# Optimization experiments

Measured on AMD Instinct MI355X. Metric: run time of the kernel, lower is better.

The kernel has to match this reference:

```python
import jax, jax.numpy as jnp
import numpy as np

H = 512
S = 65  # 64 board cells + appended constant 1


def _heads(y, wk, wq, wv):
    # y: [H, S]; wk/wq/wv: [3, H, H] -> atts: [3, S, H]
    def one(wk_i, wq_i, wv_i):
        k = wk_i @ y            # [H, S]
        q = wq_i @ y            # [H, S]
        v = wv_i @ y            # [H, S]
        sm = jax.nn.softmax(k.T @ q, axis=1)  # [S, S], softmax over dim=1
        return sm @ v.T         # [S, H]
    return jax.vmap(one)(wk, wq, wv)


def setup_inputs() -> dict:
    key = jax.random.key(0)
    ks = jax.random.split(key, 10)
    r = lambda k, s: jax.random.normal(k, s, dtype=jnp.float32)
    return {
        "inputs": r(ks[0], (1, 64)),
        "embedding": r(ks[1], (H, S)),
        "wq": r(ks[2], (3, 3, H, H)),
        "wk": r(ks[3], (3, 3, H, H)),
        "wv": r(ks[4], (3, 3, H, H)),
        "linear1": r(ks[5], (3 * H, H)),
        "linear2": r(ks[6], (3 * H, H)),
        "linear3": r(ks[7], (3 * H, 2 * H)),
        "linear4": r(ks[8], (2 * H, H)),
        "linear5": r(ks[9], (H, 64)),
    }


def reference(inputs, embedding, wq, wk, wv, linear1, linear2, linear3, linear4, linear5):
    x = jnp.concatenate([inputs[0], jnp.ones((1,), inputs.dtype)])  # [S]
    y = embedding * x  # [H, S] (broadcast over rows)

    # Layer 1 (3 heads)
    a1 = _heads(y, wk[0], wq[0], wv[0])  # [3, S, H]
    y = jax.nn.relu(jnp.concatenate([a1[0], a1[1], a1[2]], axis=1) @ linear1).T  # [H, S]

    # Layer 2 -- NOTE: original code cats att11, att12, att23 (a bug we preserve)
    a2 = _heads(y, wk[1], wq[1], wv[1])
    y = jax.nn.relu(jnp.concatenate([a1[0], a1[1], a2[2]], axis=1) @ linear2).T  # [H, S]

    # Layer 3 -- NOTE: original code cats att11, att12, att33 (preserved)
    a3 = _heads(y, wk[2], wq[2], wv[2])
    y = jax.nn.relu(jnp.concatenate([a1[0], a1[1], a3[2]], axis=1) @ linear3)[64]  # [2H]

    # dropout p=0.1 -> identity in eval mode
    y = jnp.tanh(y @ linear4)  # [H]
    score = y @ linear5        # [64]
    return score[None, :]      # [1, 64]
```

## Files before the change

### kernel.cpp

```cpp
#include <hip/hip_runtime.h>
#include <hip/hip_bf16.h>
#include <math.h>

#define H 512
#define S 65
#define SP 80
#define HS (H * S)
#define PHS (H * SP)
#define KS3 24
#define KS4 16


__global__ void scale_embed_kernel(const float* __restrict__ inp,
                                   const float* __restrict__ emb,
                                   float* __restrict__ yT) {
    int i = blockIdx.x * blockDim.x + threadIdx.x;
    if (i < PHS) {
        int s = i / H;
        int h = i % H;
        float v = 0.0f;
        if (s < S) {
            float x = (s == 64) ? 1.0f : inp[s];
            v = emb[h * S + s] * x;
        }
        yT[i] = v;
    }
}

__global__ void __launch_bounds__(256, 2)
kqv_gemm_tiled(const float* __restrict__ wq,
               const float* __restrict__ wk,
               const float* __restrict__ wv,
               int layer, int head0,
               const float* __restrict__ yT,
               float* __restrict__ part) {
    int slot  = blockIdx.z;
    int which = blockIdx.y;
    int mat = layer * 3 + head0 + slot;
    const float* W = (which == 0 ? wk : (which == 1 ? wq : wv)) + (size_t)mat * H * H;

    int n0   = (blockIdx.x & 7) * 64;
    int kidx = blockIdx.x >> 3;

    __shared__ float Wt[64 * 64];
    __shared__ float As[SP * 64];

    int t  = threadIdx.x;
    int nq = t & 15;
    int g  = t >> 4;

    float4 acc[5];
#pragma unroll
    for (int r = 0; r < 5; ++r) acc[r] = make_float4(0.f, 0.f, 0.f, 0.f);

    for (int ch = 0; ch < 4; ++ch) {
        int kc0 = kidx * 256 + ch * 64;

#pragma unroll
        for (int c = 0; c < 4; ++c) {
            int f = c * 256 + t;
            int wn  = f >> 4;
            int kf4 = f & 15;
            float4 w4 = *(const float4*)(W + (size_t)(n0 + wn) * H + kc0 + 4 * kf4);
            int sw = ((wn >> 2) ^ (kf4 & 7));
            int base = (4 * kf4) * 64 + 4 * sw + (wn & 3);
            Wt[base      ] = w4.x;
            Wt[base +  64] = w4.y;
            Wt[base + 128] = w4.z;
            Wt[base + 192] = w4.w;
        }
#pragma unroll
        for (int c = 0; c < 5; ++c) {
            int f = c * 256 + t;
            int as  = f >> 4;
            int kf4 = f & 15;
            *(float4*)(&As[as * 64 + 4 * kf4]) =
                *(const float4*)(yT + (size_t)as * H + kc0 + 4 * kf4);
        }
        __syncthreads();

#pragma unroll
        for (int k4 = 0; k4 < 16; ++k4) {
            int swc = 4 * (nq ^ (k4 & 7));
            float4 w0 = *(const float4*)(&Wt[(4 * k4 + 0) * 64 + swc]);
            float4 w1 = *(const float4*)(&Wt[(4 * k4 + 1) * 64 + swc]);
            float4 w2 = *(const float4*)(&Wt[(4 * k4 + 2) * 64 + swc]);
            float4 w3 = *(const float4*)(&Wt[(4 * k4 + 3) * 64 + swc]);
#pragma unroll
            for (int r = 0; r < 5; ++r) {
                float4 a = *(const float4*)(&As[(g + 16 * r) * 64 + 4 * k4]);
                acc[r].x = fmaf(a.x, w0.x, acc[r].x);
                acc[r].y = fmaf(a.x, w0.y, acc[r].y);
                acc[r].z = fmaf(a.x, w0.z, acc[r].z);
                acc[r].w = fmaf(a.x, w0.w, acc[r].w);
                acc[r].x = fmaf(a.y, w1.x, acc[r].x);
                acc[r].y = fmaf(a.y, w1.y, acc[r].y);
                acc[r].z = fmaf(a.y, w1.z, acc[r].z);
                acc[r].w = fmaf(a.y, w1.w, acc[r].w);
                acc[r].x = fmaf(a.z, w2.x, acc[r].x);
                acc[r].y = fmaf(a.z, w2.y, acc[r].y);
                acc[r].z = fmaf(a.z, w2.z, acc[r].z);
                acc[r].w = fmaf(a.z, w2.w, acc[r].w);
                acc[r].x = fmaf(a.w, w3.x, acc[r].x);
                acc[r].y = fmaf(a.w, w3.y, acc[r].y);
                acc[r].z = fmaf(a.w, w3.z, acc[r].z);
                acc[r].w = fmaf(a.w, w3.w, acc[r].w);
            }
        }
        __syncthreads();
    }

    float* P = part + (size_t)((slot * 3 + which) * 2 + kidx) * PHS;
#pragma unroll
    for (int r = 0; r < 5; ++r) {
        *(float4*)(P + (size_t)(g + 16 * r) * H + n0 + 4 * nq) = acc[r];
    }
}

__global__ void attn_kernel(const float* __restrict__ kqvp,
                            float* __restrict__ att) {
    int a = blockIdx.x;
    int slot = blockIdx.y;
    int tid = threadIdx.x;

    const float* K0 = kqvp + (size_t)(slot * 3 + 0) * 2 * PHS;
    const float* K1 = K0 + PHS;
    const float* Q0 = kqvp + (size_t)(slot * 3 + 1) * 2 * PHS;
    const float* Q1 = Q0 + PHS;
    const float* V0 = kqvp + (size_t)(slot * 3 + 2) * 2 * PHS;
    const float* V1 = V0 + PHS;
    float* ao = att + (size_t)slot * S * H;

    __shared__ float ka[H];
    __shared__ float smv[S];
    __shared__ float p[S];

    ka[tid]       = K0[(size_t)a * H + tid]       + K1[(size_t)a * H + tid];
    ka[tid + 256] = K0[(size_t)a * H + tid + 256] + K1[(size_t)a * H + tid + 256];
    __syncthreads();

    if (tid < S) {
        const float4* q0 = (const float4*)(Q0 + (size_t)tid * H);
        const float4* q1 = (const float4*)(Q1 + (size_t)tid * H);
        const float4* kl = (const float4*)ka;
        float4 c0 = {0,0,0,0}, c1 = {0,0,0,0};
        for (int t = 0; t < H / 4; t += 2) {
            float4 qa = q0[t],     qb = q1[t];
            float4 qc = q0[t + 1], qd = q1[t + 1];
            float4 k0 = kl[t], k1 = kl[t + 1];
            c0.x = fmaf(k0.x, qa.x + qb.x, c0.x);
            c0.y = fmaf(k0.y, qa.y + qb.y, c0.y);
            c0.z = fmaf(k0.z, qa.z + qb.z, c0.z);
            c0.w = fmaf(k0.w, qa.w + qb.w, c0.w);
            c1.x = fmaf(k1.x, qc.x + qd.x, c1.x);
            c1.y = fmaf(k1.y, qc.y + qd.y, c1.y);
            c1.z = fmaf(k1.z, qc.z + qd.z, c1.z);
            c1.w = fmaf(k1.w, qc.w + qd.w, c1.w);
        }
        smv[tid] = ((c0.x + c0.y) + (c0.z + c0.w)) + ((c1.x + c1.y) + (c1.z + c1.w));
    }
    __syncthreads();

    float maxv = -INFINITY;
    for (int i = 0; i < S; ++i) maxv = fmaxf(maxv, smv[i]);
    float sum = 0.0f;
    for (int i = 0; i < S; ++i) sum += expf(smv[i] - maxv);
    float inv = 1.0f / sum;
    if (tid < S) p[tid] = expf(smv[tid] - maxv) * inv;
    __syncthreads();

#pragma unroll
    for (int rep = 0; rep < 2; ++rep) {
        int hh = tid + rep * 256;
        float a0 = 0.f, a1 = 0.f;
#pragma unroll 4
        for (int b = 0; b < 64; b += 2) {
            a0 = fmaf(p[b    ], V0[(size_t)(b    ) * H + hh] + V1[(size_t)(b    ) * H + hh], a0);
            a1 = fmaf(p[b + 1], V0[(size_t)(b + 1) * H + hh] + V1[(size_t)(b + 1) * H + hh], a1);
        }
        a0 = fmaf(p[64], V0[(size_t)64 * H + hh] + V1[(size_t)64 * H + hh], a0);
        ao[(size_t)a * H + hh] = a0 + a1;
    }
}

__global__ void linA_kernel(const float* __restrict__ att1,
                            const float* __restrict__ lin1,
                            const float* __restrict__ lin2,
                            float* __restrict__ part1,
                            float* __restrict__ part2) {
    int seg = blockIdx.y;
    int i = blockIdx.x * blockDim.x + threadIdx.x;
    int s = i / H;
    int h = i % H;

    const float* att;
    const float* L;
    float* dst;
    if (seg < 6) {
        att = att1 + (size_t)(seg >> 1) * HS;
        L   = lin1 + (size_t)(seg * 256) * H + h;
        dst = part1 + (size_t)seg * HS;
    } else {
        int s2 = seg - 6;
        att = att1 + (size_t)(s2 >> 1) * HS;
        L   = lin2 + (size_t)(s2 * 256) * H + h;
        dst = part2 + (size_t)s2 * HS;
    }
    const float* row = att + (size_t)s * H + (seg & 1) * 256;

    float a0 = 0.f, a1 = 0.f, a2 = 0.f, a3 = 0.f;
    for (int j = 0; j < 256; j += 4) {
        a0 = fmaf(row[j + 0], L[(size_t)(j + 0) * H], a0);
        a1 = fmaf(row[j + 1], L[(size_t)(j + 1) * H], a1);
        a2 = fmaf(row[j + 2], L[(size_t)(j + 2) * H], a2);
        a3 = fmaf(row[j + 3], L[(size_t)(j + 3) * H], a3);
    }
    dst[i] = (a0 + a1) + (a2 + a3);
}

__global__ void lin2c_kernel(const float* __restrict__ att2,
                             const float* __restrict__ lin2,
                             float* __restrict__ part2) {
    int seg = 4 + blockIdx.y;
    int i = blockIdx.x * blockDim.x + threadIdx.x;
    int s = i / H;
    int h = i % H;

    const float* row = att2 + (size_t)s * H + (seg & 1) * 256;
    const float* L = lin2 + (size_t)(seg * 256) * H + h;

    float a0 = 0.f, a1 = 0.f, a2 = 0.f, a3 = 0.f;
    for (int j = 0; j < 256; j += 4) {
        a0 = fmaf(row[j + 0], L[(size_t)(j + 0) * H], a0);
        a1 = fmaf(row[j + 1], L[(size_t)(j + 1) * H], a1);
        a2 = fmaf(row[j + 2], L[(size_t)(j + 2) * H], a2);
        a3 = fmaf(row[j + 3], L[(size_t)(j + 3) * H], a3);
    }
    part2[(size_t)seg * HS + i] = (a0 + a1) + (a2 + a3);
}

__global__ void combine_relu_kernel(const float* __restrict__ part,
                                    float* __restrict__ yT) {
    int i = blockIdx.x * blockDim.x + threadIdx.x;
    if (i >= HS) return;
    float s = part[i] + part[HS + i] + part[2 * HS + i]
            + part[3 * HS + i] + part[4 * HS + i] + part[5 * HS + i];
    yT[i] = fmaxf(s, 0.0f);
}

__global__ void lin3ab_kernel(const float* __restrict__ att1,
                              const float* __restrict__ lin3,
                              float* __restrict__ tpart) {
    int j2 = blockIdx.x * 256 + threadIdx.x;
    int ks = blockIdx.y;
    const float* row = att1 + (size_t)(ks >> 3) * HS + (size_t)64 * H;
    int j0 = (ks & 7) * 64;
    int jbase = ks * 64;

    float a0 = 0.f, a1 = 0.f, a2 = 0.f, a3 = 0.f;
    for (int j = 0; j < 64; j += 4) {
        a0 = fmaf(row[j0 + j + 0], lin3[(size_t)(jbase + j + 0) * 1024 + j2], a0);
        a1 = fmaf(row[j0 + j + 1], lin3[(size_t)(jbase + j + 1) * 1024 + j2], a1);
        a2 = fmaf(row[j0 + j + 2], lin3[(size_t)(jbase + j + 2) * 1024 + j2], a2);
        a3 = fmaf(row[j0 + j + 3], lin3[(size_t)(jbase + j + 3) * 1024 + j2], a3);
    }
    tpart[ks * 1024 + j2] = (a0 + a1) + (a2 + a3);
}

__global__ void attn3_lin3c_kernel(const float* __restrict__ kqvp,
                                   const float* __restrict__ lin3,
                                   float* __restrict__ tpart) {
    int tid = threadIdx.x;
    int ks  = 16 + blockIdx.y;
    int j2  = blockIdx.x * 256 + tid;
    int j0  = (ks & 7) * 64;

    const float* K0 = kqvp;
    const float* K1 = kqvp + PHS;
    const float* Q0 = kqvp + 2 * (size_t)PHS;
    const float* Q1 = kqvp + 3 * (size_t)PHS;
    const float* V0 = kqvp + 4 * (size_t)PHS;
    const float* V1 = kqvp + 5 * (size_t)PHS;

    __shared__ float ka[H];
    __shared__ float smv[S];
    __shared__ float p[S];
    __shared__ float att_s[64];

    ka[tid]       = K0[(size_t)64 * H + tid]       + K1[(size_t)64 * H + tid];
    ka[tid + 256] = K0[(size_t)64 * H + tid + 256] + K1[(size_t)64 * H + tid + 256];
    __syncthreads();

    if (tid < S) {
        const float4* q0 = (const float4*)(Q0 + (size_t)tid * H);
        const float4* q1 = (const float4*)(Q1 + (size_t)tid * H);
        const float4* kl = (const float4*)ka;
        float4 c0 = {0,0,0,0}, c1 = {0,0,0,0};
        for (int t = 0; t < H / 4; t += 2) {
            float4 qa = q0[t],     qb = q1[t];
            float4 qc = q0[t + 1], qd = q1[t + 1];
            float4 k0 = kl[t], k1 = kl[t + 1];
            c0.x = fmaf(k0.x, qa.x + qb.x, c0.x);
            c0.y = fmaf(k0.y, qa.y + qb.y, c0.y);
            c0.z = fmaf(k0.z, qa.z + qb.z, c0.z);
            c0.w = fmaf(k0.w, qa.w + qb.w, c0.w);
            c1.x = fmaf(k1.x, qc.x + qd.x, c1.x);
            c1.y = fmaf(k1.y, qc.y + qd.y, c1.y);
            c1.z = fmaf(k1.z, qc.z + qd.z, c1.z);
            c1.w = fmaf(k1.w, qc.w + qd.w, c1.w);
        }
        smv[tid] = ((c0.x + c0.y) + (c0.z + c0.w)) + ((c1.x + c1.y) + (c1.z + c1.w));
    }
    __syncthreads();

    float maxv = -INFINITY;
    for (int i = 0; i < S; ++i) maxv = fmaxf(maxv, smv[i]);
    float sum = 0.0f;
    for (int i = 0; i < S; ++i) sum += expf(smv[i] - maxv);
    float inv = 1.0f / sum;
    if (tid < S) p[tid] = expf(smv[tid] - maxv) * inv;
    __syncthreads();

    if (tid < 64) {
        int hh = j0 + tid;
        float a0 = 0.f, a1 = 0.f;
#pragma unroll 4
        for (int b = 0; b < 64; b += 2) {
            a0 = fmaf(p[b    ], V0[(size_t)(b    ) * H + hh] + V1[(size_t)(b    ) * H + hh], a0);
            a1 = fmaf(p[b + 1], V0[(size_t)(b + 1) * H + hh] + V1[(size_t)(b + 1) * H + hh], a1);
        }
        a0 = fmaf(p[64], V0[(size_t)64 * H + hh] + V1[(size_t)64 * H + hh], a0);
        att_s[tid] = a0 + a1;
    }
    __syncthreads();

    int jbase = ks * 64;
    float a0 = 0.f, a1 = 0.f, a2 = 0.f, a3 = 0.f;
    for (int j = 0; j < 64; j += 4) {
        a0 = fmaf(att_s[j + 0], lin3[(size_t)(jbase + j + 0) * 1024 + j2], a0);
        a1 = fmaf(att_s[j + 1], lin3[(size_t)(jbase + j + 1) * 1024 + j2], a1);
        a2 = fmaf(att_s[j + 2], lin3[(size_t)(jbase + j + 2) * 1024 + j2], a2);
        a3 = fmaf(att_s[j + 3], lin3[(size_t)(jbase + j + 3) * 1024 + j2], a3);
    }
    tpart[ks * 1024 + j2] = (a0 + a1) + (a2 + a3);
}

__global__ void lin4_partial_kernel(const float* __restrict__ tpart,
                                    const float* __restrict__ lin4,
                                    float* __restrict__ upart) {
    __shared__ float tl[64];
    int hh = blockIdx.x * 256 + threadIdx.x;
    int ks = blockIdx.y;
    int j2base = ks * 64;

    if (threadIdx.x < 64) {
        int j2 = j2base + threadIdx.x;
        float s = 0.f;
#pragma unroll
        for (int p = 0; p < KS3; ++p) s += tpart[p * 1024 + j2];
        tl[threadIdx.x] = fmaxf(s, 0.f);
    }
    __syncthreads();

    float a0 = 0.f, a1 = 0.f, a2 = 0.f, a3 = 0.f;
    for (int j = 0; j < 64; j += 4) {
        a0 = fmaf(tl[j + 0], lin4[(size_t)(j2base + j + 0) * H + hh], a0);
        a1 = fmaf(tl[j + 1], lin4[(size_t)(j2base + j + 1) * H + hh], a1);
        a2 = fmaf(tl[j + 2], lin4[(size_t)(j2base + j + 2) * H + hh], a2);
        a3 = fmaf(tl[j + 3], lin4[(size_t)(j2base + j + 3) * H + hh], a3);
    }
    upart[ks * H + hh] = (a0 + a1) + (a2 + a3);
}

__global__ void final_out_kernel(const float* __restrict__ upart,
                                 const float* __restrict__ lin5,
                                 float* __restrict__ out) {
    __shared__ float u[H];
    __shared__ float pr[8][64];
    int tid = threadIdx.x;

    {
        float s = 0.f;
#pragma unroll
        for (int p = 0; p < KS4; ++p) s += upart[p * H + tid];
        u[tid] = tanhf(s);
    }
    __syncthreads();

    int o  = tid & 63;
    int sl = tid >> 6;
    float acc = 0.f;
    int h0 = sl * 64;
#pragma unroll 8
    for (int j = 0; j < 64; ++j) {
        acc = fmaf(u[h0 + j], lin5[(h0 + j) * 64 + o], acc);
    }
    pr[sl][o] = acc;
    __syncthreads();

    if (tid < 64) {
        float s = 0.f;
#pragma unroll
        for (int p = 0; p < 8; ++p) s += pr[p][tid];
        out[tid] = s;
    }
}

extern "C" void kernel_launch(void* const* d_in, const int* in_sizes, int n_in,
                              void* d_out, int out_size, void* d_ws, size_t ws_size,
                              hipStream_t stream) {
    const float* inputs  = (const float*)d_in[0];
    const float* emb     = (const float*)d_in[1];
    const float* wq      = (const float*)d_in[2];
    const float* wk      = (const float*)d_in[3];
    const float* wv      = (const float*)d_in[4];
    const float* linear1 = (const float*)d_in[5];
    const float* linear2 = (const float*)d_in[6];
    const float* linear3 = (const float*)d_in[7];
    const float* linear4 = (const float*)d_in[8];
    const float* linear5 = (const float*)d_in[9];
    float* out = (float*)d_out;

    float* ws    = (float*)d_ws;
    float* y     = ws;
    float* kqvp  = y     + PHS;
    float* att1  = kqvp  + 18 * PHS;
    float* att2  = att1  + 3 * HS;
    float* part1 = att2  + HS;
    float* part2 = part1 + 6 * HS;
    float* tpart = part2 + 6 * HS;
    float* upart = tpart + KS3 * 1024;

    const int nb  = HS / 256;
    const int nbp = PHS / 256;

    scale_embed_kernel<<<nbp, 256, 0, stream>>>(inputs, emb, y);

    kqv_gemm_tiled<<<dim3(16, 3, 3), 256, 0, stream>>>(wq, wk, wv, 0, 0, y, kqvp);
    attn_kernel<<<dim3(S, 3), 256, 0, stream>>>(kqvp, att1);
    linA_kernel<<<dim3(nb, 10), 256, 0, stream>>>(att1, linear1, linear2, part1, part2);
    lin3ab_kernel<<<dim3(4, 16), 256, 0, stream>>>(att1, linear3, tpart);
    combine_relu_kernel<<<nb, 256, 0, stream>>>(part1, y);

    kqv_gemm_tiled<<<dim3(16, 3, 1), 256, 0, stream>>>(wq, wk, wv, 1, 2, y, kqvp);
    attn_kernel<<<dim3(S, 1), 256, 0, stream>>>(kqvp, att2);
    lin2c_kernel<<<dim3(nb, 2), 256, 0, stream>>>(att2, linear2, part2);
    combine_relu_kernel<<<nb, 256, 0, stream>>>(part2, y);

    kqv_gemm_tiled<<<dim3(16, 3, 1), 256, 0, stream>>>(wq, wk, wv, 2, 2, y, kqvp);
    attn3_lin3c_kernel<<<dim3(4, 8), 256, 0, stream>>>(kqvp, linear3, tpart);

    lin4_partial_kernel<<<dim3(2, KS4), 256, 0, stream>>>(tpart, linear4, upart);
    final_out_kernel<<<1, 512, 0, stream>>>(upart, linear5, out);
}
```

Baseline: 262.2 us.

## Replace naive linear-layer kernels with shared-memory tiled GEMM and parallelize attention scores

The per-element linear1/linear2 kernels, which streamed a weight column per thread, are replaced by a shared-memory tiled GEMM that uses 64x64 weight tiles, 80-row activation tiles and register blocking, split-K into 12 partials. The lin3ab work is folded into the linear1 launch, and the combine step now sums 12 padded partials. The attention score dot products are split across all 256 threads (4 slices per key) rather than only 65 threads. This trades a larger partial-sum buffer and an extra reduction for better weight reuse and higher thread utilization.

```diff
diff --git a/kernel.cpp b/kernel.cpp
--- a/kernel.cpp
+++ b/kernel.cpp
@@ -18,7 +18,7 @@
     if (i < PHS) {
         int s = i / H;
         int h = i % H;
-        float v = 0.0f;
+        float v = 0.f;
         if (s < S) {
             float x = (s == 64) ? 1.0f : inp[s];
             v = emb[h * S + s] * x;
@@ -55,7 +55,6 @@
 
     for (int ch = 0; ch < 4; ++ch) {
         int kc0 = kidx * 256 + ch * 64;
-
 #pragma unroll
         for (int c = 0; c < 4; ++c) {
             int f = c * 256 + t;
@@ -117,21 +116,47 @@
     }
 }
 
+__device__ __forceinline__ float score_part(const float* __restrict__ Q0,
+                                            const float* __restrict__ Q1,
+                                            const float* __restrict__ ka,
+                                            int b, int t) {
+    const float4* q0 = (const float4*)(Q0 + (size_t)b * H) + t * 32;
+    const float4* q1 = (const float4*)(Q1 + (size_t)b * H) + t * 32;
+    const float4* kl = (const float4*)ka + t * 32;
+    float4 c0 = {0,0,0,0}, c1 = {0,0,0,0};
+#pragma unroll
+    for (int u = 0; u < 32; u += 2) {
+        float4 qa = q0[u], qb = q1[u], k0 = kl[u];
+        float4 qc = q0[u+1], qd = q1[u+1], k1 = kl[u+1];
+        c0.x = fmaf(k0.x, qa.x + qb.x, c0.x);
+        c0.y = fmaf(k0.y, qa.y + qb.y, c0.y);
+        c0.z = fmaf(k0.z, qa.z + qb.z, c0.z);
+        c0.w = fmaf(k0.w, qa.w + qb.w, c0.w);
+        c1.x = fmaf(k1.x, qc.x + qd.x, c1.x);
+        c1.y = fmaf(k1.y, qc.y + qd.y, c1.y);
+        c1.z = fmaf(k1.z, qc.z + qd.z, c1.z);
+        c1.w = fmaf(k1.w, qc.w + qd.w, c1.w);
+    }
+    return ((c0.x + c0.y) + (c0.z + c0.w)) + ((c1.x + c1.y) + (c1.z + c1.w));
+}
+
 __global__ void attn_kernel(const float* __restrict__ kqvp,
                             float* __restrict__ att) {
     int a = blockIdx.x;
     int slot = blockIdx.y;
     int tid = threadIdx.x;
 
-    const float* K0 = kqvp + (size_t)(slot * 3 + 0) * 2 * PHS;
-    const float* K1 = K0 + PHS;
-    const float* Q0 = kqvp + (size_t)(slot * 3 + 1) * 2 * PHS;
-    const float* Q1 = Q0 + PHS;
-    const float* V0 = kqvp + (size_t)(slot * 3 + 2) * 2 * PHS;
-    const float* V1 = V0 + PHS;
-    float* ao = att + (size_t)slot * S * H;
+    const float* base = kqvp + (size_t)slot * 6 * PHS;
+    const float* K0 = base;
+    const float* K1 = base + PHS;
+    const float* Q0 = base + 2 * (size_t)PHS;
+    const float* Q1 = base + 3 * (size_t)PHS;
+    const float* V0 = base + 4 * (size_t)PHS;
+    const float* V1 = base + 5 * (size_t)PHS;
+    float* ao = att + (size_t)slot * PHS + (size_t)a * H;
 
     __shared__ float ka[H];
+    __shared__ float sp[4 * 65];
     __shared__ float smv[S];
     __shared__ float p[S];
 
@@ -139,25 +164,16 @@
     ka[tid + 256] = K0[(size_t)a * H + tid + 256] + K1[(size_t)a * H + tid + 256];
     __syncthreads();
 
+    {
+        int b = tid & 63;
+        int t = tid >> 6;
+        sp[t * 65 + b] = score_part(Q0, Q1, ka, b, t);
+        if (tid < 4) sp[tid * 65 + 64] = score_part(Q0, Q1, ka, 64, tid);
+    }
+    __syncthreads();
+
     if (tid < S) {
-        const float4* q0 = (const float4*)(Q0 + (size_t)tid * H);
-        const float4* q1 = (const float4*)(Q1 + (size_t)tid * H);
-        const float4* kl = (const float4*)ka;
-        float4 c0 = {0,0,0,0}, c1 = {0,0,0,0};
-        for (int t = 0; t < H / 4; t += 2) {
-            float4 qa = q0[t],     qb = q1[t];
-            float4 qc = q0[t + 1], qd = q1[t + 1];
-            float4 k0 = kl[t], k1 = kl[t + 1];
-            c0.x = fmaf(k0.x, qa.x + qb.x, c0.x);
-            c0.y = fmaf(k0.y, qa.y + qb.y, c0.y);
-            c0.z = fmaf(k0.z, qa.z + qb.z, c0.z);
-            c0.w = fmaf(k0.w, qa.w + qb.w, c0.w);
-            c1.x = fmaf(k1.x, qc.x + qd.x, c1.x);
-            c1.y = fmaf(k1.y, qc.y + qd.y, c1.y);
-            c1.z = fmaf(k1.z, qc.z + qd.z, c1.z);
-            c1.w = fmaf(k1.w, qc.w + qd.w, c1.w);
-        }
-        smv[tid] = ((c0.x + c0.y) + (c0.z + c0.w)) + ((c1.x + c1.y) + (c1.z + c1.w));
+        smv[tid] = (sp[tid] + sp[65 + tid]) + (sp[130 + tid] + sp[195 + tid]);
     }
     __syncthreads();
 
@@ -179,92 +195,149 @@
             a1 = fmaf(p[b + 1], V0[(size_t)(b + 1) * H + hh] + V1[(size_t)(b + 1) * H + hh], a1);
         }
         a0 = fmaf(p[64], V0[(size_t)64 * H + hh] + V1[(size_t)64 * H + hh], a0);
-        ao[(size_t)a * H + hh] = a0 + a1;
-    }
-}
-
-__global__ void linA_kernel(const float* __restrict__ att1,
-                            const float* __restrict__ lin1,
-                            const float* __restrict__ lin2,
-                            float* __restrict__ part1,
-                            float* __restrict__ part2) {
-    int seg = blockIdx.y;
-    int i = blockIdx.x * blockDim.x + threadIdx.x;
-    int s = i / H;
-    int h = i % H;
-
-    const float* att;
-    const float* L;
-    float* dst;
-    if (seg < 6) {
-        att = att1 + (size_t)(seg >> 1) * HS;
-        L   = lin1 + (size_t)(seg * 256) * H + h;
-        dst = part1 + (size_t)seg * HS;
+        ao[hh] = a0 + a1;
+    }
+}
+
+__device__ __forceinline__ void lin_gemm_dev(const float* __restrict__ A01,
+                                             const float* __restrict__ A2,
+                                             const float* __restrict__ L,
+                                             float* __restrict__ Pbase,
+                                             int ntile, int kidx, int kbase,
+                                             int tid,
+                                             float* __restrict__ Bs,
+                                             float* __restrict__ As) {
+    int n0 = ntile * 64;
+    int nq = tid & 15;
+    int g  = tid >> 4;
+
+    float4 acc[5];
+#pragma unroll
+    for (int r = 0; r < 5; ++r) acc[r] = make_float4(0.f, 0.f, 0.f, 0.f);
+
+#pragma unroll
+    for (int ch = 0; ch < 2; ++ch) {
+        int kg = kbase + kidx * 128 + ch * 64;
+        int head = kg >> 9;
+        const float* Asrc = (head < 2) ? (A01 + (size_t)head * PHS) : A2;
+        int col0 = kg & 511;
+
+#pragma unroll
+        for (int c = 0; c < 4; ++c) {
+            int f = c * 256 + tid;
+            int kk  = f >> 4;
+            int hf4 = f & 15;
+            *(float4*)(&Bs[kk * 64 + 4 * hf4]) =
+                *(const float4*)(L + (size_t)(kg + kk) * H + n0 + 4 * hf4);
+        }
+#pragma unroll
+        for (int c = 0; c < 5; ++c) {
+            int f = c * 256 + tid;
+            int as  = f >> 4;
+            int kf4 = f & 15;
+            *(float4*)(&As[as * 68 + 4 * kf4]) =
+                *(const float4*)(Asrc + (size_t)as * H + col0 + 4 * kf4);
+        }
+        __syncthreads();
+
+#pragma unroll
+        for (int k4 = 0; k4 < 16; ++k4) {
+            float4 w0 = *(const float4*)(&Bs[(4 * k4 + 0) * 64 + 4 * nq]);
+            float4 w1 = *(const float4*)(&Bs[(4 * k4 + 1) * 64 + 4 * nq]);
+            float4 w2 = *(const float4*)(&Bs[(4 * k4 + 2) * 64 + 4 * nq]);
+            float4 w3 = *(const float4*)(&Bs[(4 * k4 + 3) * 64 + 4 * nq]);
+#pragma unroll
+            for (int r = 0; r < 5; ++r) {
+                float4 a = *(const float4*)(&As[(g + 16 * r) * 68 + 4 * k4]);
+                acc[r].x = fmaf(a.x, w0.x, acc[r].x);
+                acc[r].y = fmaf(a.x, w0.y, acc[r].y);
+                acc[r].z = fmaf(a.x, w0.z, acc[r].z);
+                acc[r].w = fmaf(a.x, w0.w, acc[r].w);
+                acc[r].x = fmaf(a.y, w1.x, acc[r].x);
+                acc[r].y = fmaf(a.y, w1.y, acc[r].y);
+                acc[r].z = fmaf(a.y, w1.z, acc[r].z);
+                acc[r].w = fmaf(a.y, w1.w, acc[r].w);
+                acc[r].x = fmaf(a.z, w2.x, acc[r].x);
+                acc[r].y = fmaf(a.z, w2.y, acc[r].y);
+                acc[r].z = fmaf(a.z, w2.z, acc[r].z);
+                acc[r].w = fmaf(a.z, w2.w, acc[r].w);
+                acc[r].x = fmaf(a.w, w3.x, acc[r].x);
+                acc[r].y = fmaf(a.w, w3.y, acc[r].y);
+                acc[r].z = fmaf(a.w, w3.z, acc[r].z);
+                acc[r].w = fmaf(a.w, w3.w, acc[r].w);
+            }
+        }
+        __syncthreads();
+    }
+
+    float* P = Pbase + (size_t)kidx * PHS;
+#pragma unroll
+    for (int r = 0; r < 5; ++r) {
+        *(float4*)(P + (size_t)(g + 16 * r) * H + n0 + 4 * nq) = acc[r];
+    }
+}
+
+__global__ void __launch_bounds__(256, 2)
+lin1plus_kernel(const float* __restrict__ att1,
+                const float* __restrict__ lin1,
+                const float* __restrict__ lin3,
+                float* __restrict__ plin1,
+                float* __restrict__ tpart) {
+    __shared__ float Bs[64 * 64];
+    __shared__ float As[SP * 68];
+    int bx = blockIdx.x;
+    int tid = threadIdx.x;
+
+    if (bx < 96) {
+        lin_gemm_dev(att1, att1 + 2 * (size_t)PHS, lin1, plin1,
+                     bx & 7, bx >> 3, 0, tid, Bs, As);
     } else {
-        int s2 = seg - 6;
-        att = att1 + (size_t)(s2 >> 1) * HS;
-        L   = lin2 + (size_t)(s2 * 256) * H + h;
-        dst = part2 + (size_t)s2 * HS;
-    }
-    const float* row = att + (size_t)s * H + (seg & 1) * 256;
-
-    float a0 = 0.f, a1 = 0.f, a2 = 0.f, a3 = 0.f;
-    for (int j = 0; j < 256; j += 4) {
-        a0 = fmaf(row[j + 0], L[(size_t)(j + 0) * H], a0);
-        a1 = fmaf(row[j + 1], L[(size_t)(j + 1) * H], a1);
-        a2 = fmaf(row[j + 2], L[(size_t)(j + 2) * H], a2);
-        a3 = fmaf(row[j + 3], L[(size_t)(j + 3) * H], a3);
-    }
-    dst[i] = (a0 + a1) + (a2 + a3);
-}
-
-__global__ void lin2c_kernel(const float* __restrict__ att2,
-                             const float* __restrict__ lin2,
-                             float* __restrict__ part2) {
-    int seg = 4 + blockIdx.y;
-    int i = blockIdx.x * blockDim.x + threadIdx.x;
-    int s = i / H;
-    int h = i % H;
-
-    const float* row = att2 + (size_t)s * H + (seg & 1) * 256;
-    const float* L = lin2 + (size_t)(seg * 256) * H + h;
-
-    float a0 = 0.f, a1 = 0.f, a2 = 0.f, a3 = 0.f;
-    for (int j = 0; j < 256; j += 4) {
-        a0 = fmaf(row[j + 0], L[(size_t)(j + 0) * H], a0);
-        a1 = fmaf(row[j + 1], L[(size_t)(j + 1) * H], a1);
-        a2 = fmaf(row[j + 2], L[(size_t)(j + 2) * H], a2);
-        a3 = fmaf(row[j + 3], L[(size_t)(j + 3) * H], a3);
-    }
-    part2[(size_t)seg * HS + i] = (a0 + a1) + (a2 + a3);
-}
-
-__global__ void combine_relu_kernel(const float* __restrict__ part,
-                                    float* __restrict__ yT) {
-    int i = blockIdx.x * blockDim.x + threadIdx.x;
-    if (i >= HS) return;
-    float s = part[i] + part[HS + i] + part[2 * HS + i]
-            + part[3 * HS + i] + part[4 * HS + i] + part[5 * HS + i];
+        int idx = bx - 96;
+        int j2 = (idx & 3) * 256 + tid;
+        int ks = idx >> 2;
+        const float* row = att1 + (size_t)(ks >> 3) * PHS + (size_t)64 * H;
+        int j0 = (ks & 7) * 64;
+        int jbase = ks * 64;
+        float a0 = 0.f, a1 = 0.f, a2 = 0.f, a3 = 0.f;
+        for (int j = 0; j < 64; j += 4) {
+            a0 = fmaf(row[j0 + j + 0], lin3[(size_t)(jbase + j + 0) * 1024 + j2], a0);
+            a1 = fmaf(row[j0 + j + 1], lin3[(size_t)(jbase + j + 1) * 1024 + j2], a1);
+            a2 = fmaf(row[j0 + j + 2], lin3[(size_t)(jbase + j + 2) * 1024 + j2], a2);
+            a3 = fmaf(row[j0 + j + 3], lin3[(size_t)(jbase + j + 3) * 1024 + j2], a3);
+        }
+        tpart[ks * 1024 + j2] = (a0 + a1) + (a2 + a3);
+    }
+}
+
+__global__ void __launch_bounds__(256, 2)
+lin2ab_kernel(const float* __restrict__ att1,
+              const float* __restrict__ lin2,
+              float* __restrict__ plin2) {
+    __shared__ float Bs[64 * 64];
+    __shared__ float As[SP * 68];
+    int bx = blockIdx.x;
+    lin_gemm_dev(att1, att1, lin2, plin2, bx & 7, bx >> 3, 0,
+                 threadIdx.x, Bs, As);
+}
+
+__global__ void __launch_bounds__(256, 2)
+lin2c_kernel(const float* __restrict__ att2,
+             const float* __restrict__ lin2,
+             float* __restrict__ plin2) {
+    __shared__ float Bs[64 * 64];
+    __shared__ float As[SP * 68];
+    int bx = blockIdx.x;
+    lin_gemm_dev(att2, att2, lin2, plin2 + 8 * (size_t)PHS,
+                 bx & 7, bx >> 3, 1024, threadIdx.x, Bs, As);
+}
+
+__global__ void combine12_relu_kernel(const float* __restrict__ part,
+                                      float* __restrict__ yT) {
+    int i = blockIdx.x * 256 + threadIdx.x;
+    float s = 0.f;
+#pragma unroll
+    for (int p = 0; p < 12; ++p) s += part[(size_t)p * PHS + i];
     yT[i] = fmaxf(s, 0.0f);
-}
-
-__global__ void lin3ab_kernel(const float* __restrict__ att1,
-                              const float* __restrict__ lin3,
-                              float* __restrict__ tpart) {
-    int j2 = blockIdx.x * 256 + threadIdx.x;
-    int ks = blockIdx.y;
-    const float* row = att1 + (size_t)(ks >> 3) * HS + (size_t)64 * H;
-    int j0 = (ks & 7) * 64;
-    int jbase = ks * 64;
-
-    float a0 = 0.f, a1 = 0.f, a2 = 0.f, a3 = 0.f;
-    for (int j = 0; j < 64; j += 4) {
-        a0 = fmaf(row[j0 + j + 0], lin3[(size_t)(jbase + j + 0) * 1024 + j2], a0);
-        a1 = fmaf(row[j0 + j + 1], lin3[(size_t)(jbase + j + 1) * 1024 + j2], a1);
-        a2 = fmaf(row[j0 + j + 2], lin3[(size_t)(jbase + j + 2) * 1024 + j2], a2);
-        a3 = fmaf(row[j0 + j + 3], lin3[(size_t)(jbase + j + 3) * 1024 + j2], a3);
-    }
-    tpart[ks * 1024 + j2] = (a0 + a1) + (a2 + a3);
 }
 
 __global__ void attn3_lin3c_kernel(const float* __restrict__ kqvp,
@@ -283,6 +356,7 @@
     const float* V1 = kqvp + 5 * (size_t)PHS;
 
     __shared__ float ka[H];
+    __shared__ float sp[4 * 65];
     __shared__ float smv[S];
     __shared__ float p[S];
     __shared__ float att_s[64];
@@ -291,25 +365,16 @@
     ka[tid + 256] = K0[(size_t)64 * H + tid + 256] + K1[(size_t)64 * H + tid + 256];
     __syncthreads();
 
+    {
+        int b = tid & 63;
+        int t = tid >> 6;
+        sp[t * 65 + b] = score_part(Q0, Q1, ka, b, t);
+        if (tid < 4) sp[tid * 65 + 64] = score_part(Q0, Q1, ka, 64, tid);
+    }
+    __syncthreads();
+
     if (tid < S) {
-        const float4* q0 = (const float4*)(Q0 + (size_t)tid * H);
-        const float4* q1 = (const float4*)(Q1 + (size_t)tid * H);
-        const float4* kl = (const float4*)ka;
-        float4 c0 = {0,0,0,0}, c1 = {0,0,0,0};
-        for (int t = 0; t < H / 4; t += 2) {
-            float4 qa = q0[t],     qb = q1[t];
-            float4 qc = q0[t + 1], qd = q1[t + 1];
-            float4 k0 = kl[t], k1 = kl[t + 1];
-            c0.x = fmaf(k0.x, qa.x + qb.x, c0.x);
-            c0.y = fmaf(k0.y, qa.y + qb.y, c0.y);
-            c0.z = fmaf(k0.z, qa.z + qb.z, c0.z);
-            c0.w = fmaf(k0.w, qa.w + qb.w, c0.w);
-            c1.x = fmaf(k1.x, qc.x + qd.x, c1.x);
-            c1.y = fmaf(k1.y, qc.y + qd.y, c1.y);
-            c1.z = fmaf(k1.z, qc.z + qd.z, c1.z);
-            c1.w = fmaf(k1.w, qc.w + qd.w, c1.w);
-        }
-        smv[tid] = ((c0.x + c0.y) + (c0.z + c0.w)) + ((c1.x + c1.y) + (c1.z + c1.w));
+        smv[tid] = (sp[tid] + sp[65 + tid]) + (sp[130 + tid] + sp[195 + tid]);
     }
     __syncthreads();
 
@@ -425,10 +490,10 @@
     float* y     = ws;
     float* kqvp  = y     + PHS;
     float* att1  = kqvp  + 18 * PHS;
-    float* att2  = att1  + 3 * HS;
-    float* part1 = att2  + HS;
-    float* part2 = part1 + 6 * HS;
-    float* tpart = part2 + 6 * HS;
+    float* att2  = att1  + 3 * PHS;
+    float* plin1 = att2  + PHS;
+    float* plin2 = plin1 + 12 * PHS;
+    float* tpart = plin2 + 12 * PHS;
     float* upart = tpart + KS3 * 1024;
 
     const int nb  = HS / 256;
@@ -438,14 +503,14 @@
 
     kqv_gemm_tiled<<<dim3(16, 3, 3), 256, 0, stream>>>(wq, wk, wv, 0, 0, y, kqvp);
     attn_kernel<<<dim3(S, 3), 256, 0, stream>>>(kqvp, att1);
-    linA_kernel<<<dim3(nb, 10), 256, 0, stream>>>(att1, linear1, linear2, part1, part2);
-    lin3ab_kernel<<<dim3(4, 16), 256, 0, stream>>>(att1, linear3, tpart);
-    combine_relu_kernel<<<nb, 256, 0, stream>>>(part1, y);
+    lin1plus_kernel<<<160, 256, 0, stream>>>(att1, linear1, linear3, plin1, tpart);
+    lin2ab_kernel<<<64, 256, 0, stream>>>(att1, linear2, plin2);
+    combine12_relu_kernel<<<nb, 256, 0, stream>>>(plin1, y);
 
     kqv_gemm_tiled<<<dim3(16, 3, 1), 256, 0, stream>>>(wq, wk, wv, 1, 2, y, kqvp);
     attn_kernel<<<dim3(S, 1), 256, 0, stream>>>(kqvp, att2);
-    lin2c_kernel<<<dim3(nb, 2), 256, 0, stream>>>(att2, linear2, part2);
-    combine_relu_kernel<<<nb, 256, 0, stream>>>(part2, y);
+    lin2c_kernel<<<32, 256, 0, stream>>>(att2, linear2, plin2);
+    combine12_relu_kernel<<<nb, 256, 0, stream>>>(plin2, y);
 
     kqv_gemm_tiled<<<dim3(16, 3, 1), 256, 0, stream>>>(wq, wk, wv, 2, 2, y, kqvp);
     attn3_lin3c_kernel<<<dim3(4, 8), 256, 0, stream>>>(kqvp, linear3, tpart);
```

New measurement: 428.7 us. 1.63x slower.
